# Kernel tuning notes

Measured on AMD Instinct MI355X. Metric: run time of the kernel, lower is better.

The kernel has to match this reference:

```python
import jax, jax.numpy as jnp
import numpy as np

B, C, H, W = 4, 256, 48, 48
HEADS, DH = 8, 32
INNER = HEADS * DH
HID = 128  # max(16, INNER//2)
SCALE = DH ** -0.5
EPS = 1e-6


def setup_inputs() -> dict:
    key = jax.random.key(0)
    ks = jax.random.split(key, 32)
    s = 0.02
    inp = {
        'x': jax.random.normal(ks[0], (B, C, H, W), jnp.float32),
        'rgb_input': jax.random.uniform(ks[1], (B, 3, H, W), jnp.float32),
        'wq': jax.random.normal(ks[2], (INNER, C), jnp.float32) * s,
        'bq': jnp.zeros((INNER,), jnp.float32),
        'wk': jax.random.normal(ks[3], (INNER, C), jnp.float32) * s,
        'bk': jnp.zeros((INNER,), jnp.float32),
        'wv': jax.random.normal(ks[4], (INNER, C), jnp.float32) * s,
        'bv': jnp.zeros((INNER,), jnp.float32),
        'wproj': jax.random.normal(ks[5], (C, INNER), jnp.float32) * s,
        'bproj': jnp.zeros((C,), jnp.float32),
        'c1_w': jax.random.normal(ks[6], (HID, 1, 3, 3), jnp.float32) * s,
        'c1_b': jnp.zeros((HID,), jnp.float32),
        'c2_w': jax.random.normal(ks[7], (HID, HID, 3, 3), jnp.float32) * s,
        'c2_b': jnp.zeros((HID,), jnp.float32),
        'gq_w': jax.random.normal(ks[8], (INNER, HID), jnp.float32) * s,
        'gq_b': jnp.ones((INNER,), jnp.float32),
        'bqf_w': jax.random.normal(ks[9], (INNER, HID), jnp.float32) * s,
        'bqf_b': jnp.zeros((INNER,), jnp.float32),
        'gk_w': jax.random.normal(ks[10], (INNER, HID), jnp.float32) * s,
        'gk_b': jnp.ones((INNER,), jnp.float32),
        'bkf_w': jax.random.normal(ks[11], (INNER, HID), jnp.float32) * s,
        'bkf_b': jnp.zeros((INNER,), jnp.float32),
        'gv_w': jax.random.normal(ks[12], (INNER, HID), jnp.float32) * s,
        'gv_b': jnp.ones((INNER,), jnp.float32),
        'bvf_w': jax.random.normal(ks[13], (INNER, HID), jnp.float32) * s,
        'bvf_b': jnp.zeros((INNER,), jnp.float32),
        'alpha': jnp.float32(0.1),
    }
    return inp


def _conv3(x, w, b):
    y = jax.lax.conv_general_dilated(x, w, (1, 1), 'SAME',
                                     dimension_numbers=('NCHW', 'OIHW', 'NCHW'))
    return y + b[None, :, None, None]


def _rgb_to_luma(rgb):
    y = 0.299 * rgb[:, 0:1] + 0.587 * rgb[:, 1:2] + 0.114 * rgb[:, 2:3]
    y_min = jnp.min(y, axis=(2, 3), keepdims=True)
    y_max = jnp.max(y, axis=(2, 3), keepdims=True)
    return (y - y_min) / (y_max - y_min + EPS)


def reference(x, rgb_input, wq, bq, wk, bk, wv, bv, wproj, bproj,
              c1_w, c1_b, c2_w, c2_b,
              gq_w, gq_b, bqf_w, bqf_b, gk_w, gk_b, bkf_w, bkf_b,
              gv_w, gv_b, bvf_w, bvf_b, alpha):
    Bx, Cx, Hx, Wx = x.shape
    N = Hx * Wx
    luma = _rgb_to_luma(rgb_input)  # [B,1,H,W]

    # LumaCond trunk + FiLM params (1x1 convs then global spatial mean)
    h = jax.nn.relu(_conv3(luma, c1_w, c1_b))
    h = jax.nn.relu(_conv3(h, c2_w, c2_b))
    hm = h.mean(axis=(2, 3))  # [B,HID] (mean commutes with 1x1 conv)

    def film_params(gw, gb, bw, bb):
        g = hm @ gw.T + gb  # [B, INNER]
        bta = hm @ bw.T + bb
        return (g.reshape(Bx, HEADS, DH, 1), bta.reshape(Bx, HEADS, DH, 1))

    gq, fbq = film_params(gq_w, gq_b, bqf_w, bqf_b)
    gk, fbk = film_params(gk_w, gk_b, bkf_w, bkf_b)
    gv, fbv = film_params(gv_w, gv_b, bvf_w, bvf_b)

    def proj_film(w, b, g, bta):
        t = jnp.einsum('bchw,oc->bohw', x, w) + b[None, :, None, None]
        t = t.reshape(Bx, HEADS, DH, N)
        return g * t + bta  # [B,heads,dh,N]

    q = proj_film(wq, bq, gq, fbq)
    k = proj_film(wk, bk, gk, fbk)
    v = proj_film(wv, bv, gv, fbv)

    logits = jnp.einsum('bhdn,bhdm->bhnm', q, k) * SCALE  # [B,heads,N,N]

    # luma bias: avg-pooled inverse luma, mean-centered per image
    invL = 1.0 - luma
    invL = jax.lax.reduce_window(invL, 0.0, jax.lax.add,
                                 (1, 1, 3, 3), (1, 1, 1, 1), 'SAME') / 9.0
    invL = invL.reshape(Bx, N)
    invL = invL - invL.mean(axis=-1, keepdims=True)
    logits = logits + alpha * invL[:, None, None, :]

    attn = jax.nn.softmax(logits, axis=-1)
    out = jnp.einsum('bhnm,bhdm->bhdn', attn, v)  # [B,heads,dh,N]
    out = out.reshape(Bx, INNER, Hx, Wx)
    return jnp.einsum('bchw,oc->bohw', out, wproj) + bproj[None, :, None, None]
```

## Files before the change

kernel.cpp:

```cpp
#include <hip/hip_runtime.h>


#define NSP 2304
#define WID 48

typedef __attribute__((ext_vector_type(4))) float  fvec4;
typedef __attribute__((ext_vector_type(2))) unsigned int uvec2;
typedef __attribute__((ext_vector_type(4))) unsigned int uvec4;
typedef __attribute__((ext_vector_type(8))) short  short8;
typedef __attribute__((ext_vector_type(4))) float  f32x4;

__device__ inline unsigned short f2bf(float f){
  unsigned int u = __builtin_bit_cast(unsigned int, f);
  u += 0x7fffu + ((u >> 16) & 1u);
  return (unsigned short)(u >> 16);
}
__device__ inline unsigned pack2bf(float a, float b){
#if __has_builtin(__builtin_amdgcn_cvt_pk_bf16_f32)
  typedef __attribute__((ext_vector_type(2))) __bf16 bf16x2;
  bf16x2 r = __builtin_amdgcn_cvt_pk_bf16_f32(a, b);
  return __builtin_bit_cast(unsigned, r);
#else
  return (unsigned)f2bf(a) | ((unsigned)f2bf(b) << 16);
#endif
}

__global__ void k0b_wcast(const float* __restrict__ c2w, const float* __restrict__ wq,
                          const float* __restrict__ wk, const float* __restrict__ wv_,
                          const float* __restrict__ wproj,
                          unsigned short* __restrict__ wtb,
                          unsigned short* __restrict__ wqkvb,
                          unsigned short* __restrict__ wprojb){
  int idx = blockIdx.x*256 + threadIdx.x;
  if (idx < 147456){
    int ic = idx & 127, rem = idx >> 7;
    int oc = rem & 127, tap = rem >> 7;
    wtb[idx] = f2bf(c2w[(oc*128 + ic)*9 + tap]);
  } else if (idx < 344064){
    int j = idx - 147456;
    int mat = j >> 16, oc_ = j & 65535;
    const float* src = (mat == 0) ? wq : (mat == 1) ? wk : wv_;
    wqkvb[j] = f2bf(src[oc_]);
  } else {
    int j = idx - 344064;
    wprojb[j] = f2bf(wproj[j]);
  }
}

__global__ __launch_bounds__(256) void k0xt(const float* __restrict__ x,
                                            unsigned short* __restrict__ xt){
  int nt = blockIdx.x, cc = blockIdx.y, b = blockIdx.z, t = threadIdx.x;
  __shared__ unsigned short tb[64*72];
  int cl0 = t >> 4;
  int nl0 = (t & 15) * 4;
  #pragma unroll
  for (int ps = 0; ps < 4; ++ps){
    int cl = cl0 + ps*16;
    fvec4 v = *(const fvec4*)(x + ((size_t)(b*256 + cc*64 + cl))*NSP + nt*64 + nl0);
    #pragma unroll
    for (int i = 0; i < 4; ++i) tb[(nl0+i)*72 + cl] = f2bf(v[i]);
  }
  __syncthreads();
  int nl = t >> 2, cg = (t & 3) * 16;
  uvec4 u0 = *(const uvec4*)&tb[nl*72 + cg];
  uvec4 u1 = *(const uvec4*)&tb[nl*72 + cg + 8];
  unsigned short* dst = xt + ((size_t)(b*NSP + nt*64 + nl))*256 + cc*64 + cg;
  *(uvec4*)dst = u0;
  *(uvec4*)(dst + 8) = u1;
}

__global__ void k1_luma(const float* __restrict__ rgb, const float* __restrict__ alphaP,
                        float* __restrict__ luma_n, float* __restrict__ bias_a,
                        float* __restrict__ hm_sum){
  int b = blockIdx.x, t = threadIdx.x;
  int wv = t >> 6, lane = t & 63;
  __shared__ float ll[NSP];
  __shared__ float red[8];
  const float* rp = rgb + b*3*NSP;
  float ly[9];
  float lmin = 1e30f, lmax = -1e30f;
  #pragma unroll
  for (int ii = 0; ii < 9; ++ii){
    int i = t + 256*ii;
    float y = 0.299f*rp[i] + 0.587f*rp[NSP+i] + 0.114f*rp[2*NSP+i];
    ly[ii] = y; lmin = fminf(lmin, y); lmax = fmaxf(lmax, y);
  }
  #pragma unroll
  for (int o2 = 1; o2 < 64; o2 <<= 1){
    lmin = fminf(lmin, __shfl_xor(lmin, o2, 64));
    lmax = fmaxf(lmax, __shfl_xor(lmax, o2, 64));
  }
  if (lane == 0){ red[wv] = lmin; red[4+wv] = lmax; }
  if (t < 128) hm_sum[b*128 + t] = 0.f;
  __syncthreads();
  float mn = fminf(fminf(red[0], red[1]), fminf(red[2], red[3]));
  float mx = fmaxf(fmaxf(red[4], red[5]), fmaxf(red[6], red[7]));
  float inv = 1.0f / (mx - mn + 1e-6f);
  #pragma unroll
  for (int ii = 0; ii < 9; ++ii){
    int i = t + 256*ii;
    float v = (ly[ii] - mn) * inv;
    ll[i] = v;
    luma_n[b*NSP + i] = v;
  }
  __syncthreads();
  float pr[9]; float psum = 0.f;
  #pragma unroll
  for (int ii = 0; ii < 9; ++ii){
    int n = t + 256*ii;
    int row = n / WID, col = n - row*WID;
    float s = 0.f;
    #pragma unroll
    for (int dy = -1; dy <= 1; ++dy)
      #pragma unroll
      for (int dx = -1; dx <= 1; ++dx){
        int r2 = row+dy, c2 = col+dx;
        if (r2 >= 0 && r2 < WID && c2 >= 0 && c2 < WID) s += 1.0f - ll[r2*WID + c2];
      }
    pr[ii] = s * (1.f/9.f);
    psum += pr[ii];
  }
  #pragma unroll
  for (int o2 = 1; o2 < 64; o2 <<= 1) psum += __shfl_xor(psum, o2, 64);
  if (lane == 0) red[wv] = psum;
  __syncthreads();
  float mean = (red[0] + red[1] + red[2] + red[3]) * (1.f/(float)NSP);
  float alpha = alphaP[0] * 1.4426950408889634f;
  #pragma unroll
  for (int ii = 0; ii < 9; ++ii){
    int n = t + 256*ii;
    bias_a[b*NSP + n] = alpha * (pr[ii] - mean);
  }
}

__global__ void k2_conv1(const float* __restrict__ luma_n, const float* __restrict__ c1w,
                         const float* __restrict__ c1b, unsigned short* __restrict__ h1p){
  int nt = blockIdx.x, ocg = blockIdx.y, b = blockIdx.z, t = threadIdx.x;
  __shared__ float wsm[32*9];
  __shared__ float bsm[32];
  for (int i = t; i < 288; i += 256) wsm[i] = c1w[ocg*288 + i];
  if (t < 32) bsm[t] = c1b[ocg*32 + t];
  __syncthreads();
  int n = nt*256 + t;
  int row = n / WID, col = n - row*WID;
  const float* lp = luma_n + b*NSP;
  float lv[9];
  int k = 0;
  #pragma unroll
  for (int dy = -1; dy <= 1; ++dy)
    #pragma unroll
    for (int dx = -1; dx <= 1; ++dx, ++k){
      int r2 = row+dy, c2 = col+dx;
      lv[k] = (r2 >= 0 && r2 < WID && c2 >= 0 && c2 < WID) ? lp[r2*WID + c2] : 0.f;
    }
  unsigned int packed[16];
  #pragma unroll
  for (int oc2 = 0; oc2 < 16; ++oc2){
    float a0 = bsm[oc2*2], a1 = bsm[oc2*2+1];
    #pragma unroll
    for (int q = 0; q < 9; ++q){
      a0 += wsm[(oc2*2)*9 + q] * lv[q];
      a1 += wsm[(oc2*2+1)*9 + q] * lv[q];
    }
    packed[oc2] = pack2bf(fmaxf(a0, 0.f), fmaxf(a1, 0.f));
  }
  unsigned short* dst = h1p + ((size_t)(b*2500 + (row+1)*50 + (col+1)))*128 + ocg*32;
  #pragma unroll
  for (int q4 = 0; q4 < 4; ++q4)
    *(uvec4*)(dst + q4*8) = *(uvec4*)&packed[q4*4];
}

__global__ __launch_bounds__(256) void k3_conv2(const unsigned short* __restrict__ h1p,
    const unsigned short* __restrict__ wtb, const float* __restrict__ c2b,
    float* __restrict__ hm_sum){
  int row = blockIdx.x, mh = blockIdx.y, b = blockIdx.z;
  int t = threadIdx.x, wv = t >> 6, lane = t & 63;
  int lq = lane >> 4, lc = lane & 15;
  int ocb = mh*64 + wv*16;
  const f32x4 z4 = {0.f, 0.f, 0.f, 0.f};
  f32x4 C[3] = {z4, z4, z4};
  const unsigned short* hbase = h1p + (size_t)b*2500*128;
  #pragma unroll
  for (int tap = 0; tap < 9; ++tap){
    int dy = tap/3 - 1, dx = tap%3 - 1;
    const unsigned short* wrow = wtb + (tap*128 + ocb + lc)*128 + lq*8;
    const unsigned short* hrow = hbase + ((row+dy+1)*50 + (dx+1) + lc)*128 + lq*8;
    #pragma unroll
    for (int kc = 0; kc < 4; ++kc){
      short8 aW = *(const short8*)(wrow + kc*32);
      #pragma unroll
      for (int ntp = 0; ntp < 3; ++ntp){
        short8 bH = *(const short8*)(hrow + ntp*16*128 + kc*32);
        C[ntp] = __builtin_amdgcn_mfma_f32_16x16x32_bf16(aW, bH, C[ntp], 0, 0, 0);
      }
    }
  }
  float s[4];
  #pragma unroll
  for (int r = 0; r < 4; ++r){
    float bias = c2b[ocb + lq*4 + r];
    float v = 0.f;
    #pragma unroll
    for (int ntp = 0; ntp < 3; ++ntp) v += fmaxf(C[ntp][r] + bias, 0.f);
    v += __shfl_xor(v, 1, 64);
    v += __shfl_xor(v, 2, 64);
    v += __shfl_xor(v, 4, 64);
    v += __shfl_xor(v, 8, 64);
    s[r] = v;
  }
  if (lc == 0){
    #pragma unroll
    for (int r = 0; r < 4; ++r)
      atomicAdd(&hm_sum[b*128 + ocb + lq*4 + r], s[r]);
  }
}

__global__ void k4_film(const float* __restrict__ hm_sum,
  const float* w0, const float* b0, const float* w1, const float* b1,
  const float* w2, const float* b2, const float* w3, const float* b3,
  const float* w4, const float* b4, const float* w5, const float* b5,
  float* __restrict__ film){
  __shared__ float hs[128];
  int bb = blockIdx.x & 3, m6 = blockIdx.x >> 2, t = threadIdx.x;
  if (t < 128) hs[t] = hm_sum[bb*128 + t] * (1.f/(float)NSP);
  __syncthreads();
  const float* wm[6] = {w0,w1,w2,w3,w4,w5};
  const float* bm[6] = {b0,b1,b2,b3,b4,b5};
  const float* w = wm[m6];
  const float* bv6 = bm[m6];
  int oi = t >> 3, hi = t & 7;
  float hreg[16];
  #pragma unroll
  for (int q = 0; q < 16; ++q) hreg[q] = hs[hi*16 + q];
  #pragma unroll
  for (int pass = 0; pass < 8; ++pass){
    int o = pass*32 + oi;
    const float* wr = w + o*128 + hi*16;
    float p = 0.f;
    #pragma unroll
    for (int q4 = 0; q4 < 4; ++q4){
      fvec4 w4v = *(const fvec4*)(wr + q4*4);
      p += hreg[q4*4+0]*w4v[0] + hreg[q4*4+1]*w4v[1]
         + hreg[q4*4+2]*w4v[2] + hreg[q4*4+3]*w4v[3];
    }
    p += __shfl_xor(p, 1, 64);
    p += __shfl_xor(p, 2, 64);
    p += __shfl_xor(p, 4, 64);
    if (hi == 0) film[blockIdx.x*256 + o] = p + bv6[o];
  }
}

__global__ __launch_bounds__(256) void k5_qkv(const unsigned short* __restrict__ xt,
    const unsigned short* __restrict__ wqkvb,
    const float* __restrict__ bq, const float* __restrict__ bk, const float* __restrict__ bv,
    const float* __restrict__ film,
    unsigned short* __restrict__ q_t, unsigned short* __restrict__ k_t,
    unsigned short* __restrict__ v_b){
  int nt = blockIdx.x, ot = blockIdx.y, b = blockIdx.z;
  int t = threadIdx.x, wv = t >> 6, lane = t & 63;
  int lq = lane >> 4, lc = lane & 15;
  int p = ot >> 1;
  int omb = (ot & 1)*128 + wv*32;
  const unsigned short* wb = wqkvb + p*65536;
  const f32x4 z4 = {0.f, 0.f, 0.f, 0.f};
  f32x4 acc[2][4];
  #pragma unroll
  for (int oh = 0; oh < 2; ++oh)
    #pragma unroll
    for (int nq = 0; nq < 4; ++nq) acc[oh][nq] = z4;
  for (int kc = 0; kc < 8; ++kc){
    short8 aW[2];
    #pragma unroll
    for (int oh = 0; oh < 2; ++oh)
      aW[oh] = *(const short8*)(wb + (omb + oh*16 + lc)*256 + kc*32 + lq*8);
    short8 bX[4];
    #pragma unroll
    for (int nq = 0; nq < 4; ++nq)
      bX[nq] = *(const short8*)(xt + ((size_t)(b*NSP + nt*64 + nq*16 + lc))*256 + kc*32 + lq*8);
    #pragma unroll
    for (int oh = 0; oh < 2; ++oh)
      #pragma unroll
      for (int nq = 0; nq < 4; ++nq)
        acc[oh][nq] = __builtin_amdgcn_mfma_f32_16x16x32_bf16(aW[oh], bX[nq], acc[oh][nq], 0, 0, 0);
  }
  const float* bvec = (p == 0) ? bq : (p == 1) ? bk : bv;
  int hq = omb >> 5;
  unsigned short* qk = (p == 0) ? q_t : k_t;
  #pragma unroll
  for (int oh = 0; oh < 2; ++oh){
    fvec4 g4 = *(const fvec4*)(film + (2*p*4 + b)*256 + omb + oh*16 + lq*4);
    fvec4 t4 = *(const fvec4*)(film + ((2*p+1)*4 + b)*256 + omb + oh*16 + lq*4);
    fvec4 z4b = *(const fvec4*)(bvec + omb + oh*16 + lq*4);
    #pragma unroll
    for (int nq = 0; nq < 4; ++nq){
      int n = nt*64 + nq*16 + lc;
      float v0 = g4[0]*(acc[oh][nq][0] + z4b[0]) + t4[0];
      float v1 = g4[1]*(acc[oh][nq][1] + z4b[1]) + t4[1];
      float v2 = g4[2]*(acc[oh][nq][2] + z4b[2]) + t4[2];
      float v3 = g4[3]*(acc[oh][nq][3] + z4b[3]) + t4[3];
      if (p == 0){
        const float sc = 0.17677669529663687f * 1.4426950408889634f;
        v0 *= sc; v1 *= sc; v2 *= sc; v3 *= sc;
      }
      if (p < 2){
        uvec2 u;
        u.x = pack2bf(v0, v1);
        u.y = pack2bf(v2, v3);
        *(uvec2*)(qk + ((size_t)((b*8 + hq)*NSP + n))*32 + oh*16 + lq*4) = u;
      } else {
        int om = omb + oh*16 + lq*4;
        v_b[((size_t)(b*256 + om + 0))*NSP + n] = f2bf(v0);
        v_b[((size_t)(b*256 + om + 1))*NSP + n] = f2bf(v1);
        v_b[((size_t)(b*256 + om + 2))*NSP + n] = f2bf(v2);
        v_b[((size_t)(b*256 + om + 3))*NSP + n] = f2bf(v3);
      }
    }
  }
}

__global__ __launch_bounds__(256) void k6_attn(const unsigned short* __restrict__ q_t,
    const unsigned short* __restrict__ k_t, const unsigned short* __restrict__ v_b,
    const float* __restrict__ bias_a,
    unsigned short* __restrict__ o0, unsigned short* __restrict__ o1,
    unsigned short* __restrict__ o2, unsigned short* __restrict__ o3,
    float* __restrict__ l0, float* __restrict__ l1,
    float* __restrict__ l2, float* __restrict__ l3){
  int bx = blockIdx.x, h = blockIdx.y, b = blockIdx.z;
  int qblk = bx >> 2, s = bx & 3;
  unsigned short* op = (s == 0) ? o0 : (s == 1) ? o1 : (s == 2) ? o2 : o3;
  float* lp = (s == 0) ? l0 : (s == 1) ? l1 : (s == 2) ? l2 : l3;
  int t = threadIdx.x, wv = t >> 6, lane = t & 63;
  int lq = lane >> 4, lc = lane & 15;
  int bh = b*8 + h;
  int nb0 = qblk*128 + wv*32;
  const f32x4 z4 = {0.f, 0.f, 0.f, 0.f};
  __shared__ float ps[4][512];
  float* myps = ps[wv];
  int xm = (lc & 7) << 2;
  int wbase = lc*32;
  const uvec4 onesu = {0x3F803F80u, 0x3F803F80u, 0x3F803F80u, 0x3F803F80u};
  const short8 aOnes = __builtin_bit_cast(short8, onesu);
  short8 aQ[2];
  #pragma unroll
  for (int qf = 0; qf < 2; ++qf)
    aQ[qf] = *(const short8*)(q_t + ((size_t)(bh*NSP + nb0 + qf*16 + lc))*32 + lq*8);
  f32x4 O[2][2];
  f32x4 Ol[2];
  #pragma unroll
  for (int qf = 0; qf < 2; ++qf){
    Ol[qf] = z4;
    #pragma unroll
    for (int dh = 0; dh < 2; ++dh) O[qf][dh] = z4;
  }
  const float* brow = bias_a + b*NSP;
  int ms = s*576;

  for (int it = 0; it < 9; ++it){
    int m0 = ms + it*64;
    short8 aK[4]; fvec4 c0[4]; short8 aV[2][2];
    #pragma unroll
    for (int g = 0; g < 4; ++g)
      aK[g] = *(const short8*)(k_t + ((size_t)(bh*NSP + m0 + g*16 + lc))*32 + lq*8);
    #pragma unroll
    for (int g = 0; g < 4; ++g)
      c0[g] = *(const fvec4*)(brow + m0 + g*16 + lq*4);
    #pragma unroll
    for (int dh = 0; dh < 2; ++dh)
      #pragma unroll
      for (int mh = 0; mh < 2; ++mh)
        aV[dh][mh] = *(const short8*)(v_b + ((size_t)(b*256 + h*32 + dh*16 + lc))*NSP + m0 + mh*32 + lq*8);
    #pragma unroll
    for (int qf = 0; qf < 2; ++qf){
      #pragma unroll
      for (int g = 0; g < 4; ++g){
        f32x4 S = __builtin_amdgcn_mfma_f32_16x16x32_bf16(aK[g], aQ[qf], c0[g], 0, 0, 0);
        uvec2 w2;
        w2.x = pack2bf(__builtin_amdgcn_exp2f(S[0]), __builtin_amdgcn_exp2f(S[1]));
        w2.y = pack2bf(__builtin_amdgcn_exp2f(S[2]), __builtin_amdgcn_exp2f(S[3]));
        int kp = g*8 + lq*2;
        *(uvec2*)&myps[wbase + (kp ^ xm)] = w2;
      }
      #pragma unroll
      for (int mh = 0; mh < 2; ++mh){
        int rb = (mh*16 + lq*4) ^ xm;
        uvec4 up = *(const uvec4*)&myps[wbase + rb];
        short8 bP = __builtin_bit_cast(short8, up);
        Ol[qf] = __builtin_amdgcn_mfma_f32_16x16x32_bf16(aOnes, bP, Ol[qf], 0, 0, 0);
        #pragma unroll
        for (int dh = 0; dh < 2; ++dh)
          O[qf][dh] = __builtin_amdgcn_mfma_f32_16x16x32_bf16(aV[dh][mh], bP, O[qf][dh], 0, 0, 0);
      }
    }
  }
  #pragma unroll
  for (int qf = 0; qf < 2; ++qf){
    int nidx = nb0 + qf*16 + lc;
    if (lq == 0) lp[b*NSP + nidx] = Ol[qf][0];
    #pragma unroll
    for (int dh = 0; dh < 2; ++dh){
      uvec2 u;
      u.x = pack2bf(O[qf][dh][0], O[qf][dh][1]);
      u.y = pack2bf(O[qf][dh][2], O[qf][dh][3]);
      *(uvec2*)(op + ((size_t)(b*NSP + nidx))*256 + h*32 + dh*16 + lq*4) = u;
    }
  }
}

__global__ __launch_bounds__(256) void k7_proj(const unsigned short* __restrict__ a0,
    const unsigned short* __restrict__ a1, const unsigned short* __restrict__ a2,
    const unsigned short* __restrict__ a3,
    const float* __restrict__ l0p, const float* __restrict__ l1p,
    const float* __restrict__ l2p, const float* __restrict__ l3p,
    const unsigned short* __restrict__ wprojb,
    const float* __restrict__ bproj, float* __restrict__ out){
  int nt = blockIdx.x, ct = blockIdx.y, b = blockIdx.z;
  int t = threadIdx.x, wv = t >> 6, lane = t & 63;
  int lq = lane >> 4, lc = lane & 15;
  __shared__ float rls[32];
  if (t < 32){
    int gi = b*NSP + nt*32 + t;
    rls[t] = 1.0f / (l0p[gi] + l1p[gi] + l2p[gi] + l3p[gi]);
  }
  __syncthreads();
  int cb = ct*128 + wv*32;
  const f32x4 z4 = {0.f, 0.f, 0.f, 0.f};
  f32x4 acc[2][2];
  #pragma unroll
  for (int ch = 0; ch < 2; ++ch)
    #pragma unroll
    for (int nq = 0; nq < 2; ++nq) acc[ch][nq] = z4;
  const unsigned short* srcs[4] = {a0, a1, a2, a3};
  for (int kc = 0; kc < 8; ++kc){
    short8 aW[2];
    #pragma unroll
    for (int ch = 0; ch < 2; ++ch)
      aW[ch] = *(const short8*)(wprojb + (cb + ch*16 + lc)*256 + kc*32 + lq*8);
    #pragma unroll
    for (int src = 0; src < 4; ++src){
      const unsigned short* ap = srcs[src];
      short8 bA[2];
      #pragma unroll
      for (int nq = 0; nq < 2; ++nq)
        bA[nq] = *(const short8*)(ap + ((size_t)(b*NSP + nt*32 + nq*16 + lc))*256 + kc*32 + lq*8);
      #pragma unroll
      for (int ch = 0; ch < 2; ++ch)
        #pragma unroll
        for (int nq = 0; nq < 2; ++nq)
          acc[ch][nq] = __builtin_amdgcn_mfma_f32_16x16x32_bf16(aW[ch], bA[nq], acc[ch][nq], 0, 0, 0);
    }
  }
  #pragma unroll
  for (int ch = 0; ch < 2; ++ch){
    #pragma unroll
    for (int nq = 0; nq < 2; ++nq){
      int n = nt*32 + nq*16 + lc;
      float rl = rls[nq*16 + lc];
      #pragma unroll
      for (int r = 0; r < 4; ++r){
        int c = cb + ch*16 + lq*4 + r;
        out[((size_t)(b*256 + c))*NSP + n] = acc[ch][nq][r]*rl + bproj[c];
      }
    }
  }
}

extern "C" void kernel_launch(void* const* d_in, const int* in_sizes, int n_in,
                              void* d_out, int out_size, void* d_ws, size_t ws_size,
                              hipStream_t stream) {
  const float* x     = (const float*)d_in[0];
  const float* rgb   = (const float*)d_in[1];
  const float* wq    = (const float*)d_in[2];
  const float* bq    = (const float*)d_in[3];
  const float* wk    = (const float*)d_in[4];
  const float* bk    = (const float*)d_in[5];
  const float* wv    = (const float*)d_in[6];
  const float* bv    = (const float*)d_in[7];
  const float* wproj = (const float*)d_in[8];
  const float* bproj = (const float*)d_in[9];
  const float* c1w   = (const float*)d_in[10];
  const float* c1b   = (const float*)d_in[11];
  const float* c2w   = (const float*)d_in[12];
  const float* c2b   = (const float*)d_in[13];
  const float* gq_w  = (const float*)d_in[14];
  const float* gq_b  = (const float*)d_in[15];
  const float* bqf_w = (const float*)d_in[16];
  const float* bqf_b = (const float*)d_in[17];
  const float* gk_w  = (const float*)d_in[18];
  const float* gk_b  = (const float*)d_in[19];
  const float* bkf_w = (const float*)d_in[20];
  const float* bkf_b = (const float*)d_in[21];
  const float* gv_w  = (const float*)d_in[22];
  const float* gv_b  = (const float*)d_in[23];
  const float* bvf_w = (const float*)d_in[24];
  const float* bvf_b = (const float*)d_in[25];
  const float* alphaP= (const float*)d_in[26];

  char* w = (char*)d_ws;
  float* luma_n = (float*)w;            w += 4*NSP*4;
  float* bias_a = (float*)w;            w += 4*NSP*4;
  float* hm_sum = (float*)w;            w += 512*4;
  float* film   = (float*)w;            w += 6*4*256*4;
  unsigned short* h1p = (unsigned short*)w; w += 4*2500*128*2;
  unsigned short* wtb = (unsigned short*)w; w += 9*128*128*2;
  unsigned short* wqkvb = (unsigned short*)w; w += 3*256*256*2;
  unsigned short* wprojb = (unsigned short*)w; w += 256*256*2;
  unsigned short* xt  = (unsigned short*)w; w += (size_t)4*NSP*256*2;
  unsigned short* q_t = (unsigned short*)w; w += (size_t)4*8*NSP*32*2;
  unsigned short* k_t = (unsigned short*)w; w += (size_t)4*8*NSP*32*2;
  unsigned short* v_b = (unsigned short*)w; w += (size_t)4*256*NSP*2;
  unsigned short* o_part[4];
  for (int i = 0; i < 4; ++i){ o_part[i] = (unsigned short*)w; w += (size_t)4*NSP*256*2; }
  float* l_part[4];
  for (int i = 0; i < 4; ++i){ l_part[i] = (float*)w; w += 4*NSP*4; }

  (void)hipMemsetAsync(h1p, 0, (size_t)4*2500*128*2, stream);
  k0b_wcast<<<1600, 256, 0, stream>>>(c2w, wq, wk, wv, wproj, wtb, wqkvb, wprojb);
  k0xt    <<<dim3(36,4,4), 256, 0, stream>>>(x, xt);
  k1_luma <<<4, 256, 0, stream>>>(rgb, alphaP, luma_n, bias_a, hm_sum);
  k2_conv1<<<dim3(9,4,4), 256, 0, stream>>>(luma_n, c1w, c1b, h1p);
  k3_conv2<<<dim3(48,2,4), 256, 0, stream>>>(h1p, wtb, c2b, hm_sum);
  k4_film <<<24, 256, 0, stream>>>(hm_sum, gq_w, gq_b, bqf_w, bqf_b,
                                   gk_w, gk_b, bkf_w, bkf_b,
                                   gv_w, gv_b, bvf_w, bvf_b, film);
  k5_qkv  <<<dim3(36,6,4), 256, 0, stream>>>(xt, wqkvb, bq, bk, bv, film,
                                             q_t, k_t, v_b);
  k6_attn <<<dim3(72,8,4), 256, 0, stream>>>(q_t, k_t, v_b, bias_a,
                                             o_part[0], o_part[1], o_part[2], o_part[3],
                                             l_part[0], l_part[1], l_part[2], l_part[3]);
  k7_proj <<<dim3(72,2,4), 256, 0, stream>>>(o_part[0], o_part[1], o_part[2], o_part[3],
                                             l_part[0], l_part[1], l_part[2], l_part[3],
                                             wprojb, bproj, (float*)d_out);
}
```

Measured before the change: 302.4 us.

## Merge prep kernels, fold FiLM into QKV, and prefetch attention tiles

Folds the memset, weight cast, x transpose and luma kernels into one block-dispatched prep launch. The FiLM parameter matvec moves into the QKV kernel, where each block computes its own gamma/beta in shared memory, and the film buffer is dropped. The attention inner loop now double-buffers the next K/bias/V register tile while the current one is computed. The aim is to cut launch count and hide global load latency in attention, at the cost of redundant FiLM work across QKV blocks and higher register pressure.

```diff
diff --git a/kernel.cpp b/kernel.cpp
--- a/kernel.cpp
+++ b/kernel.cpp
@@ -25,112 +25,126 @@
 #endif
 }
 
-__global__ void k0b_wcast(const float* __restrict__ c2w, const float* __restrict__ wq,
-                          const float* __restrict__ wk, const float* __restrict__ wv_,
-                          const float* __restrict__ wproj,
-                          unsigned short* __restrict__ wtb,
-                          unsigned short* __restrict__ wqkvb,
-                          unsigned short* __restrict__ wprojb){
-  int idx = blockIdx.x*256 + threadIdx.x;
-  if (idx < 147456){
-    int ic = idx & 127, rem = idx >> 7;
-    int oc = rem & 127, tap = rem >> 7;
-    wtb[idx] = f2bf(c2w[(oc*128 + ic)*9 + tap]);
-  } else if (idx < 344064){
-    int j = idx - 147456;
-    int mat = j >> 16, oc_ = j & 65535;
-    const float* src = (mat == 0) ? wq : (mat == 1) ? wk : wv_;
-    wqkvb[j] = f2bf(src[oc_]);
-  } else {
-    int j = idx - 344064;
-    wprojb[j] = f2bf(wproj[j]);
-  }
-}
-
-__global__ __launch_bounds__(256) void k0xt(const float* __restrict__ x,
-                                            unsigned short* __restrict__ xt){
-  int nt = blockIdx.x, cc = blockIdx.y, b = blockIdx.z, t = threadIdx.x;
-  __shared__ unsigned short tb[64*72];
-  int cl0 = t >> 4;
-  int nl0 = (t & 15) * 4;
-  #pragma unroll
-  for (int ps = 0; ps < 4; ++ps){
-    int cl = cl0 + ps*16;
-    fvec4 v = *(const fvec4*)(x + ((size_t)(b*256 + cc*64 + cl))*NSP + nt*64 + nl0);
-    #pragma unroll
-    for (int i = 0; i < 4; ++i) tb[(nl0+i)*72 + cl] = f2bf(v[i]);
-  }
-  __syncthreads();
-  int nl = t >> 2, cg = (t & 3) * 16;
-  uvec4 u0 = *(const uvec4*)&tb[nl*72 + cg];
-  uvec4 u1 = *(const uvec4*)&tb[nl*72 + cg + 8];
-  unsigned short* dst = xt + ((size_t)(b*NSP + nt*64 + nl))*256 + cc*64 + cg;
-  *(uvec4*)dst = u0;
-  *(uvec4*)(dst + 8) = u1;
-}
-
-__global__ void k1_luma(const float* __restrict__ rgb, const float* __restrict__ alphaP,
-                        float* __restrict__ luma_n, float* __restrict__ bias_a,
-                        float* __restrict__ hm_sum){
-  int b = blockIdx.x, t = threadIdx.x;
-  int wv = t >> 6, lane = t & 63;
-  __shared__ float ll[NSP];
-  __shared__ float red[8];
-  const float* rp = rgb + b*3*NSP;
-  float ly[9];
-  float lmin = 1e30f, lmax = -1e30f;
-  #pragma unroll
-  for (int ii = 0; ii < 9; ++ii){
-    int i = t + 256*ii;
-    float y = 0.299f*rp[i] + 0.587f*rp[NSP+i] + 0.114f*rp[2*NSP+i];
-    ly[ii] = y; lmin = fminf(lmin, y); lmax = fmaxf(lmax, y);
-  }
-  #pragma unroll
-  for (int o2 = 1; o2 < 64; o2 <<= 1){
-    lmin = fminf(lmin, __shfl_xor(lmin, o2, 64));
-    lmax = fmaxf(lmax, __shfl_xor(lmax, o2, 64));
-  }
-  if (lane == 0){ red[wv] = lmin; red[4+wv] = lmax; }
-  if (t < 128) hm_sum[b*128 + t] = 0.f;
-  __syncthreads();
-  float mn = fminf(fminf(red[0], red[1]), fminf(red[2], red[3]));
-  float mx = fmaxf(fmaxf(red[4], red[5]), fmaxf(red[6], red[7]));
-  float inv = 1.0f / (mx - mn + 1e-6f);
-  #pragma unroll
-  for (int ii = 0; ii < 9; ++ii){
-    int i = t + 256*ii;
-    float v = (ly[ii] - mn) * inv;
-    ll[i] = v;
-    luma_n[b*NSP + i] = v;
-  }
-  __syncthreads();
-  float pr[9]; float psum = 0.f;
-  #pragma unroll
-  for (int ii = 0; ii < 9; ++ii){
-    int n = t + 256*ii;
-    int row = n / WID, col = n - row*WID;
-    float s = 0.f;
-    #pragma unroll
-    for (int dy = -1; dy <= 1; ++dy)
-      #pragma unroll
-      for (int dx = -1; dx <= 1; ++dx){
-        int r2 = row+dy, c2 = col+dx;
-        if (r2 >= 0 && r2 < WID && c2 >= 0 && c2 < WID) s += 1.0f - ll[r2*WID + c2];
-      }
-    pr[ii] = s * (1.f/9.f);
-    psum += pr[ii];
-  }
-  #pragma unroll
-  for (int o2 = 1; o2 < 64; o2 <<= 1) psum += __shfl_xor(psum, o2, 64);
-  if (lane == 0) red[wv] = psum;
-  __syncthreads();
-  float mean = (red[0] + red[1] + red[2] + red[3]) * (1.f/(float)NSP);
-  float alpha = alphaP[0] * 1.4426950408889634f;
-  #pragma unroll
-  for (int ii = 0; ii < 9; ++ii){
-    int n = t + 256*ii;
-    bias_a[b*NSP + n] = alpha * (pr[ii] - mean);
-  }
+__global__ __launch_bounds__(256) void kprep(
+    const float* __restrict__ rgb, const float* __restrict__ alphaP,
+    const float* __restrict__ x,
+    const float* __restrict__ c2w, const float* __restrict__ wq,
+    const float* __restrict__ wk, const float* __restrict__ wv_,
+    const float* __restrict__ wproj,
+    float* __restrict__ luma_n, float* __restrict__ bias_a,
+    float* __restrict__ hm_sum,
+    unsigned short* __restrict__ xt,
+    unsigned short* __restrict__ wtb, unsigned short* __restrict__ wqkvb,
+    unsigned short* __restrict__ wprojb, unsigned short* __restrict__ h1p){
+  __shared__ __align__(16) float smemf[2368];
+  int bx = blockIdx.x, t = threadIdx.x;
+
+  if (bx < 4){
+    int b = bx, wv = t >> 6, lane = t & 63;
+    float* ll = smemf;
+    float* red = smemf + NSP;
+    const float* rp = rgb + b*3*NSP;
+    float ly[9];
+    float lmin = 1e30f, lmax = -1e30f;
+    #pragma unroll
+    for (int ii = 0; ii < 9; ++ii){
+      int i = t + 256*ii;
+      float y = 0.299f*rp[i] + 0.587f*rp[NSP+i] + 0.114f*rp[2*NSP+i];
+      ly[ii] = y; lmin = fminf(lmin, y); lmax = fmaxf(lmax, y);
+    }
+    #pragma unroll
+    for (int o2 = 1; o2 < 64; o2 <<= 1){
+      lmin = fminf(lmin, __shfl_xor(lmin, o2, 64));
+      lmax = fmaxf(lmax, __shfl_xor(lmax, o2, 64));
+    }
+    if (lane == 0){ red[wv] = lmin; red[4+wv] = lmax; }
+    if (t < 128) hm_sum[b*128 + t] = 0.f;
+    __syncthreads();
+    float mn = fminf(fminf(red[0], red[1]), fminf(red[2], red[3]));
+    float mx = fmaxf(fmaxf(red[4], red[5]), fmaxf(red[6], red[7]));
+    float inv = 1.0f / (mx - mn + 1e-6f);
+    #pragma unroll
+    for (int ii = 0; ii < 9; ++ii){
+      int i = t + 256*ii;
+      float v = (ly[ii] - mn) * inv;
+      ll[i] = v;
+      luma_n[b*NSP + i] = v;
+    }
+    __syncthreads();
+    float pr[9]; float psum = 0.f;
+    #pragma unroll
+    for (int ii = 0; ii < 9; ++ii){
+      int n = t + 256*ii;
+      int row = n / WID, col = n - row*WID;
+      float s = 0.f;
+      #pragma unroll
+      for (int dy = -1; dy <= 1; ++dy)
+        #pragma unroll
+        for (int dx = -1; dx <= 1; ++dx){
+          int r2 = row+dy, c2 = col+dx;
+          if (r2 >= 0 && r2 < WID && c2 >= 0 && c2 < WID) s += 1.0f - ll[r2*WID + c2];
+        }
+      pr[ii] = s * (1.f/9.f);
+      psum += pr[ii];
+    }
+    #pragma unroll
+    for (int o2 = 1; o2 < 64; o2 <<= 1) psum += __shfl_xor(psum, o2, 64);
+    if (lane == 0) red[wv] = psum;
+    __syncthreads();
+    float mean = (red[0] + red[1] + red[2] + red[3]) * (1.f/(float)NSP);
+    float alpha = alphaP[0] * 1.4426950408889634f;
+    #pragma unroll
+    for (int ii = 0; ii < 9; ++ii){
+      int n = t + 256*ii;
+      bias_a[b*NSP + n] = alpha * (pr[ii] - mean);
+    }
+    return;
+  }
+
+  if (bx < 580){
+    int idx = bx - 4;
+    int nt = idx % 36, cc = (idx/36) & 3, b = idx/144;
+    unsigned short* tb = (unsigned short*)smemf;
+    int cl0 = t >> 4;
+    int nl0 = (t & 15) * 4;
+    #pragma unroll
+    for (int ps = 0; ps < 4; ++ps){
+      int cl = cl0 + ps*16;
+      fvec4 v = *(const fvec4*)(x + ((size_t)(b*256 + cc*64 + cl))*NSP + nt*64 + nl0);
+      #pragma unroll
+      for (int i = 0; i < 4; ++i) tb[(nl0+i)*72 + cl] = f2bf(v[i]);
+    }
+    __syncthreads();
+    int nl = t >> 2, cg = (t & 3) * 16;
+    uvec4 u0 = *(const uvec4*)&tb[nl*72 + cg];
+    uvec4 u1 = *(const uvec4*)&tb[nl*72 + cg + 8];
+    unsigned short* dst = xt + ((size_t)(b*NSP + nt*64 + nl))*256 + cc*64 + cg;
+    *(uvec4*)dst = u0;
+    *(uvec4*)(dst + 8) = u1;
+    return;
+  }
+
+  if (bx < 2180){
+    int idx = (bx - 580)*256 + t;
+    if (idx < 147456){
+      int ic = idx & 127, rem = idx >> 7;
+      int oc = rem & 127, tap = rem >> 7;
+      wtb[idx] = f2bf(c2w[(oc*128 + ic)*9 + tap]);
+    } else if (idx < 344064){
+      int j = idx - 147456;
+      int mat = j >> 16, oc_ = j & 65535;
+      const float* src = (mat == 0) ? wq : (mat == 1) ? wk : wv_;
+      wqkvb[j] = f2bf(src[oc_]);
+    } else {
+      int j = idx - 344064;
+      wprojb[j] = f2bf(wproj[j]);
+    }
+    return;
+  }
+
+  int idx = (bx - 2180)*256 + t;
+  uvec4 z = {0u, 0u, 0u, 0u};
+  ((uvec4*)h1p)[idx] = z;
 }
 
 __global__ void k2_conv1(const float* __restrict__ luma_n, const float* __restrict__ c1w,
@@ -215,51 +229,46 @@
   }
 }
 
-__global__ void k4_film(const float* __restrict__ hm_sum,
-  const float* w0, const float* b0, const float* w1, const float* b1,
-  const float* w2, const float* b2, const float* w3, const float* b3,
-  const float* w4, const float* b4, const float* w5, const float* b5,
-  float* __restrict__ film){
-  __shared__ float hs[128];
-  int bb = blockIdx.x & 3, m6 = blockIdx.x >> 2, t = threadIdx.x;
-  if (t < 128) hs[t] = hm_sum[bb*128 + t] * (1.f/(float)NSP);
-  __syncthreads();
-  const float* wm[6] = {w0,w1,w2,w3,w4,w5};
-  const float* bm[6] = {b0,b1,b2,b3,b4,b5};
-  const float* w = wm[m6];
-  const float* bv6 = bm[m6];
-  int oi = t >> 3, hi = t & 7;
-  float hreg[16];
-  #pragma unroll
-  for (int q = 0; q < 16; ++q) hreg[q] = hs[hi*16 + q];
-  #pragma unroll
-  for (int pass = 0; pass < 8; ++pass){
-    int o = pass*32 + oi;
-    const float* wr = w + o*128 + hi*16;
-    float p = 0.f;
-    #pragma unroll
-    for (int q4 = 0; q4 < 4; ++q4){
-      fvec4 w4v = *(const fvec4*)(wr + q4*4);
-      p += hreg[q4*4+0]*w4v[0] + hreg[q4*4+1]*w4v[1]
-         + hreg[q4*4+2]*w4v[2] + hreg[q4*4+3]*w4v[3];
-    }
-    p += __shfl_xor(p, 1, 64);
-    p += __shfl_xor(p, 2, 64);
-    p += __shfl_xor(p, 4, 64);
-    if (hi == 0) film[blockIdx.x*256 + o] = p + bv6[o];
-  }
-}
-
-__global__ __launch_bounds__(256) void k5_qkv(const unsigned short* __restrict__ xt,
+__global__ __launch_bounds__(256) void k45_qkv(const unsigned short* __restrict__ xt,
     const unsigned short* __restrict__ wqkvb,
     const float* __restrict__ bq, const float* __restrict__ bk, const float* __restrict__ bv,
-    const float* __restrict__ film,
+    const float* __restrict__ hm_sum,
+    const float* __restrict__ gq_w, const float* __restrict__ gq_b,
+    const float* __restrict__ bqf_w, const float* __restrict__ bqf_b,
+    const float* __restrict__ gk_w, const float* __restrict__ gk_b,
+    const float* __restrict__ bkf_w, const float* __restrict__ bkf_b,
+    const float* __restrict__ gv_w, const float* __restrict__ gv_b,
+    const float* __restrict__ bvf_w, const float* __restrict__ bvf_b,
     unsigned short* __restrict__ q_t, unsigned short* __restrict__ k_t,
     unsigned short* __restrict__ v_b){
   int nt = blockIdx.x, ot = blockIdx.y, b = blockIdx.z;
   int t = threadIdx.x, wv = t >> 6, lane = t & 63;
   int lq = lane >> 4, lc = lane & 15;
   int p = ot >> 1;
+  __shared__ float hs[128];
+  __shared__ float fg[128];
+  __shared__ float fb[128];
+  if (t < 128) hs[t] = hm_sum[b*128 + t] * (1.f/(float)NSP);
+  __syncthreads();
+  {
+    int o_l = t & 127;
+    int o = (ot & 1)*128 + o_l;
+    const float* gw  = (p==0) ? gq_w : (p==1) ? gk_w : gv_w;
+    const float* gb  = (p==0) ? gq_b : (p==1) ? gk_b : gv_b;
+    const float* bw  = (p==0) ? bqf_w : (p==1) ? bkf_w : bvf_w;
+    const float* bb  = (p==0) ? bqf_b : (p==1) ? bkf_b : bvf_b;
+    const float* w_  = (t < 128) ? gw : bw;
+    float a = (t < 128) ? gb[o] : bb[o];
+    const float* wr = w_ + o*128;
+    #pragma unroll
+    for (int h2 = 0; h2 < 128; h2 += 4){
+      fvec4 w4 = *(const fvec4*)(wr + h2);
+      a += hs[h2]*w4[0] + hs[h2+1]*w4[1] + hs[h2+2]*w4[2] + hs[h2+3]*w4[3];
+    }
+    if (t < 128) fg[o_l] = a; else fb[o_l] = a;
+  }
+  __syncthreads();
+
   int omb = (ot & 1)*128 + wv*32;
   const unsigned short* wb = wqkvb + p*65536;
   const f32x4 z4 = {0.f, 0.f, 0.f, 0.f};
@@ -288,8 +297,9 @@
   unsigned short* qk = (p == 0) ? q_t : k_t;
   #pragma unroll
   for (int oh = 0; oh < 2; ++oh){
-    fvec4 g4 = *(const fvec4*)(film + (2*p*4 + b)*256 + omb + oh*16 + lq*4);
-    fvec4 t4 = *(const fvec4*)(film + ((2*p+1)*4 + b)*256 + omb + oh*16 + lq*4);
+    int lo = wv*32 + oh*16 + lq*4;
+    fvec4 g4 = *(fvec4*)&fg[lo];
+    fvec4 t4 = *(fvec4*)&fb[lo];
     fvec4 z4b = *(const fvec4*)(bvec + omb + oh*16 + lq*4);
     #pragma unroll
     for (int nq = 0; nq < 4; ++nq){
@@ -352,33 +362,31 @@
     #pragma unroll
     for (int dh = 0; dh < 2; ++dh) O[qf][dh] = z4;
   }
-  const float* brow = bias_a + b*NSP;
   int ms = s*576;
-
-  for (int it = 0; it < 9; ++it){
-    int m0 = ms + it*64;
-    short8 aK[4]; fvec4 c0[4]; short8 aV[2][2];
-    #pragma unroll
-    for (int g = 0; g < 4; ++g)
-      aK[g] = *(const short8*)(k_t + ((size_t)(bh*NSP + m0 + g*16 + lc))*32 + lq*8);
-    #pragma unroll
-    for (int g = 0; g < 4; ++g)
-      c0[g] = *(const fvec4*)(brow + m0 + g*16 + lq*4);
-    #pragma unroll
-    for (int dh = 0; dh < 2; ++dh)
-      #pragma unroll
-      for (int mh = 0; mh < 2; ++mh)
-        aV[dh][mh] = *(const short8*)(v_b + ((size_t)(b*256 + h*32 + dh*16 + lc))*NSP + m0 + mh*32 + lq*8);
+  const unsigned short* kp  = k_t + ((size_t)(bh*NSP + ms + lc))*32 + lq*8;
+  const float*          bp  = bias_a + b*NSP + ms + lq*4;
+  const unsigned short* vp0 = v_b + ((size_t)(b*256 + h*32 + lc))*NSP + ms + lq*8;
+  const unsigned short* vp1 = vp0 + (size_t)16*NSP;
+
+  short8 aK[4]; fvec4 c0[4]; short8 aV[2][2];
+  #pragma unroll
+  for (int g = 0; g < 4; ++g) aK[g] = *(const short8*)(kp + g*512);
+  #pragma unroll
+  for (int g = 0; g < 4; ++g) c0[g] = *(const fvec4*)(bp + g*16);
+  aV[0][0] = *(const short8*)(vp0); aV[0][1] = *(const short8*)(vp0 + 32);
+  aV[1][0] = *(const short8*)(vp1); aV[1][1] = *(const short8*)(vp1 + 32);
+
+  auto compute = [&](const short8 cK[4], const fvec4 cc0[4], const short8 cV[2][2]){
     #pragma unroll
     for (int qf = 0; qf < 2; ++qf){
       #pragma unroll
       for (int g = 0; g < 4; ++g){
-        f32x4 S = __builtin_amdgcn_mfma_f32_16x16x32_bf16(aK[g], aQ[qf], c0[g], 0, 0, 0);
+        f32x4 S = __builtin_amdgcn_mfma_f32_16x16x32_bf16(cK[g], aQ[qf], cc0[g], 0, 0, 0);
         uvec2 w2;
         w2.x = pack2bf(__builtin_amdgcn_exp2f(S[0]), __builtin_amdgcn_exp2f(S[1]));
         w2.y = pack2bf(__builtin_amdgcn_exp2f(S[2]), __builtin_amdgcn_exp2f(S[3]));
-        int kp = g*8 + lq*2;
-        *(uvec2*)&myps[wbase + (kp ^ xm)] = w2;
+        int kp2 = g*8 + lq*2;
+        *(uvec2*)&myps[wbase + (kp2 ^ xm)] = w2;
       }
       #pragma unroll
       for (int mh = 0; mh < 2; ++mh){
@@ -388,10 +396,29 @@
         Ol[qf] = __builtin_amdgcn_mfma_f32_16x16x32_bf16(aOnes, bP, Ol[qf], 0, 0, 0);
         #pragma unroll
         for (int dh = 0; dh < 2; ++dh)
-          O[qf][dh] = __builtin_amdgcn_mfma_f32_16x16x32_bf16(aV[dh][mh], bP, O[qf][dh], 0, 0, 0);
+          O[qf][dh] = __builtin_amdgcn_mfma_f32_16x16x32_bf16(cV[dh][mh], bP, O[qf][dh], 0, 0, 0);
       }
     }
-  }
+  };
+
+  #pragma unroll 1
+  for (int it = 0; it < 8; ++it){
+    kp += 2048; bp += 64; vp0 += 64; vp1 += 64;
+    short8 nK[4]; fvec4 nc[4]; short8 nV[2][2];
+    #pragma unroll
+    for (int g = 0; g < 4; ++g) nK[g] = *(const short8*)(kp + g*512);
+    #pragma unroll
+    for (int g = 0; g < 4; ++g) nc[g] = *(const fvec4*)(bp + g*16);
+    nV[0][0] = *(const short8*)(vp0); nV[0][1] = *(const short8*)(vp0 + 32);
+    nV[1][0] = *(const short8*)(vp1); nV[1][1] = *(const short8*)(vp1 + 32);
+    compute(aK, c0, aV);
+    #pragma unroll
+    for (int g = 0; g < 4; ++g){ aK[g] = nK[g]; c0[g] = nc[g]; }
+    aV[0][0] = nV[0][0]; aV[0][1] = nV[0][1];
+    aV[1][0] = nV[1][0]; aV[1][1] = nV[1][1];
+  }
+  compute(aK, c0, aV);
+
   #pragma unroll
   for (int qf = 0; qf < 2; ++qf){
     int nidx = nb0 + qf*16 + lc;
@@ -499,7 +526,6 @@
   float* luma_n = (float*)w;            w += 4*NSP*4;
   float* bias_a = (float*)w;            w += 4*NSP*4;
   float* hm_sum = (float*)w;            w += 512*4;
-  float* film   = (float*)w;            w += 6*4*256*4;
   unsigned short* h1p = (unsigned short*)w; w += 4*2500*128*2;
   unsigned short* wtb = (unsigned short*)w; w += 9*128*128*2;
   unsigned short* wqkvb = (unsigned short*)w; w += 3*256*256*2;
@@ -513,21 +539,20 @@
   float* l_part[4];
   for (int i = 0; i < 4; ++i){ l_part[i] = (float*)w; w += 4*NSP*4; }
 
-  (void)hipMemsetAsync(h1p, 0, (size_t)4*2500*128*2, stream);
-  k0b_wcast<<<1600, 256, 0, stream>>>(c2w, wq, wk, wv, wproj, wtb, wqkvb, wprojb);
-  k0xt    <<<dim3(36,4,4), 256, 0, stream>>>(x, xt);
-  k1_luma <<<4, 256, 0, stream>>>(rgb, alphaP, luma_n, bias_a, hm_sum);
+  kprep  <<<2805, 256, 0, stream>>>(rgb, alphaP, x, c2w, wq, wk, wv, wproj,
+                                    luma_n, bias_a, hm_sum, xt,
+                                    wtb, wqkvb, wprojb, h1p);
   k2_conv1<<<dim3(9,4,4), 256, 0, stream>>>(luma_n, c1w, c1b, h1p);
   k3_conv2<<<dim3(48,2,4), 256, 0, stream>>>(h1p, wtb, c2b, hm_sum);
-  k4_film <<<24, 256, 0, stream>>>(hm_sum, gq_w, gq_b, bqf_w, bqf_b,
-                                   gk_w, gk_b, bkf_w, bkf_b,
-                                   gv_w, gv_b, bvf_w, bvf_b, film);
-  k5_qkv  <<<dim3(36,6,4), 256, 0, stream>>>(xt, wqkvb, bq, bk, bv, film,
-                                             q_t, k_t, v_b);
-  k6_attn <<<dim3(72,8,4), 256, 0, stream>>>(q_t, k_t, v_b, bias_a,
-                                             o_part[0], o_part[1], o_part[2], o_part[3],
-                                             l_part[0], l_part[1], l_part[2], l_part[3]);
-  k7_proj <<<dim3(72,2,4), 256, 0, stream>>>(o_part[0], o_part[1], o_part[2], o_part[3],
-                                             l_part[0], l_part[1], l_part[2], l_part[3],
-                                             wprojb, bproj, (float*)d_out);
-}
+  k45_qkv<<<dim3(36,6,4), 256, 0, stream>>>(xt, wqkvb, bq, bk, bv, hm_sum,
+                                            gq_w, gq_b, bqf_w, bqf_b,
+                                            gk_w, gk_b, bkf_w, bkf_b,
+                                            gv_w, gv_b, bvf_w, bvf_b,
+                                            q_t, k_t, v_b);
+  k6_attn<<<dim3(72,8,4), 256, 0, stream>>>(q_t, k_t, v_b, bias_a,
+                                            o_part[0], o_part[1], o_part[2], o_part[3],
+                                            l_part[0], l_part[1], l_part[2], l_part[3]);
+  k7_proj<<<dim3(72,2,4), 256, 0, stream>>>(o_part[0], o_part[1], o_part[2], o_part[3],
+                                            l_part[0], l_part[1], l_part[2], l_part[3],
+                                            wprojb, bproj, (float*)d_out);
+}
```

Measured after the change: 304.5 us. Within noise of the previous version (+0.7%).
